# Kernel optimization log

Hardware: AMD Instinct MI355X
Metric: run time of the kernel (lower is better)

The kernel has to match this reference:

```python
import jax, jax.numpy as jnp
import numpy as np
from jax import lax


def _gru(x, h, Wih, Whh, bih, bhh):
    # PyTorch GRU cell: gates order (r, z, n)
    gi = x @ Wih.T + bih
    gh = h @ Whh.T + bhh
    ir, iz, inn = jnp.split(gi, 3, axis=-1)
    hr, hz, hn = jnp.split(gh, 3, axis=-1)
    r = jax.nn.sigmoid(ir + hr)
    z = jax.nn.sigmoid(iz + hz)
    n = jnp.tanh(inn + r * hn)
    return (1.0 - z) * n + z * h


def setup_inputs() -> dict:
    key = jax.random.key(0)
    ks = jax.random.split(key, 20)
    B, T, D, H, V, S = 128, 80, 4096, 1024, 6000, 10
    s = 0.02
    inp = {
        "data": jax.random.normal(ks[0], (B, T, D), dtype=jnp.float32),
        "mask": jnp.ones((B, S), dtype=jnp.float32),
        "target": jax.random.randint(ks[1], (B, S), 0, V),
        "sent_len": S,
        "enc_Wih": jax.random.normal(ks[2], (3 * H, D), dtype=jnp.float32) * s,
        "enc_Whh": jax.random.normal(ks[3], (3 * H, H), dtype=jnp.float32) * s,
        "enc_bih": jax.random.normal(ks[4], (3 * H,), dtype=jnp.float32) * s,
        "enc_bhh": jax.random.normal(ks[5], (3 * H,), dtype=jnp.float32) * s,
        "dec_Wih": jax.random.normal(ks[6], (3 * H, H), dtype=jnp.float32) * s,
        "dec_Whh": jax.random.normal(ks[7], (3 * H, H), dtype=jnp.float32) * s,
        "dec_bih": jax.random.normal(ks[8], (3 * H,), dtype=jnp.float32) * s,
        "dec_bhh": jax.random.normal(ks[9], (3 * H,), dtype=jnp.float32) * s,
        "lin1_W": jax.random.normal(ks[10], (H, 2 * H), dtype=jnp.float32) * s,
        "lin1_b": jnp.zeros((H,), dtype=jnp.float32),
        "lin2_W": jax.random.normal(ks[11], (V, H), dtype=jnp.float32) * s,
        "lin2_b": jnp.zeros((V,), dtype=jnp.float32),
        "embed": jax.random.normal(ks[12], (V, H), dtype=jnp.float32) * s,
    }
    return inp


def reference(data, mask, target, sent_len,
              enc_Wih, enc_Whh, enc_bih, enc_bhh,
              dec_Wih, dec_Whh, dec_bih, dec_bhh,
              lin1_W, lin1_b, lin2_W, lin2_b, embed):
    B = data.shape[0]
    H = lin1_b.shape[0]
    W1a = lin1_W[:, :H]   # acts on encoder hidden half
    W1b = lin1_W[:, H:]   # acts on embedded word half

    eh0 = jnp.zeros((B, H), dtype=data.dtype)
    dh0 = jnp.zeros((B, H), dtype=data.dtype)

    # ---- encode phase: feed video features; decoder sees [enc_hid, 0] ----
    def enc_step(carry, x_t):
        eh, dh = carry
        eh = _gru(x_t, eh, enc_Wih, enc_Whh, enc_bih, enc_bhh)
        u = jax.nn.relu(eh @ W1a.T + lin1_b)  # zeros half contributes nothing
        dh = _gru(u, dh, dec_Wih, dec_Whh, dec_bih, dec_bhh)
        return (eh, dh), None

    (eh, dh), _ = lax.scan(enc_step, (eh0, dh0), jnp.swapaxes(data, 0, 1))

    # ---- decode phase: encoder input is zeros; decoder sees [enc_hid, embed(word)] ----
    ir0, iz0, in0 = jnp.split(enc_bih, 3)  # zero-input encoder gates

    def dec_step(carry, tgt_t):
        eh, dh, word = carry
        gh = eh @ enc_Whh.T + enc_bhh
        hr, hz, hn = jnp.split(gh, 3, axis=-1)
        r = jax.nn.sigmoid(ir0 + hr)
        z = jax.nn.sigmoid(iz0 + hz)
        n = jnp.tanh(in0 + r * hn)
        eh = (1.0 - z) * n + z * eh

        emb = embed[word]  # [B, H]
        u = jax.nn.relu(eh @ W1a.T + emb @ W1b.T + lin1_b)
        dh = _gru(u, dh, dec_Wih, dec_Whh, dec_bih, dec_bhh)
        logp = jax.nn.log_softmax(dh @ lin2_W.T + lin2_b, axis=-1)  # [B, V]
        new_word = jnp.argmax(logp, axis=1).astype(jnp.int32)
        loss_t = -jnp.mean(logp[jnp.arange(B), tgt_t])  # NLLLoss (mask unused, as in source)
        return (eh, dh, new_word), (loss_t, new_word[0], new_word[1])

    word0 = jnp.ones((B,), dtype=jnp.int32)
    (_, _, _), (losses, sent, sent2) = lax.scan(dec_step, (eh, dh, word0), jnp.swapaxes(target, 0, 1))
    return jnp.sum(losses), sent, sent2
```

## Files before the change

### kernel.cpp

```cpp
#include <hip/hip_runtime.h>
#include <math.h>
#include <float.h>

#define B_ 128
#define T_ 80
#define D_ 4096
#define H_ 1024
#define V_ 6000
#define VP 6016
#define S_ 10
#define G3 (3*H_)
#define KSPLIT 4
#define NBLK 256
#define BAR_MASTER 320
#define BAR_GEN    336

typedef unsigned short ushort_t;
typedef unsigned long long ull_t;
typedef __attribute__((ext_vector_type(8))) short s16x8;
typedef __attribute__((ext_vector_type(4))) float fx4;

__device__ float    g_gi[(size_t)B_*T_*G3];
__device__ ushort_t g_Ah[(size_t)B_*T_*D_];
__device__ ushort_t g_Al[(size_t)B_*T_*D_];
__device__ ushort_t g_Bh[(size_t)G3*D_];
__device__ ushort_t g_Bl[(size_t)G3*D_];
__device__ ushort_t g_Whh_h[G3*H_],  g_Whh_l[G3*H_];
__device__ ushort_t g_dWih_h[G3*H_], g_dWih_l[G3*H_];
__device__ ushort_t g_dWhh_h[G3*H_], g_dWhh_l[G3*H_];
__device__ ushort_t g_l1h[H_*2*H_],  g_l1l[H_*2*H_];
__device__ ushort_t g_l2h[(size_t)VP*H_], g_l2l[(size_t)VP*H_];
__device__ float g_ghp [KSPLIT*B_*G3];
__device__ float g_gi2p[KSPLIT*B_*G3];
__device__ float g_gh2p[KSPLIT*B_*G3];
__device__ float g_up  [KSPLIT*B_*H_];
__device__ float g_eh[B_*H_];
__device__ float g_dh[B_*H_];
__device__ ushort_t g_ehh[B_*H_], g_ehl[B_*H_];
__device__ ushort_t g_dhh[B_*H_], g_dhl[B_*H_];
__device__ ushort_t g_uh[B_*H_],  g_ul[B_*H_];
__device__ ushort_t g_cath[B_*2*H_], g_catl[B_*2*H_];
__device__ float g_logitsp[2*B_*VP];
__device__ int   g_word[B_];
__device__ int   g_bar[512];

__device__ __forceinline__ ull_t ald64(const void* p) {
    return __hip_atomic_load((const ull_t*)p, __ATOMIC_RELAXED, __HIP_MEMORY_SCOPE_AGENT);
}
__device__ __forceinline__ void ast64(void* p, ull_t v) {
    __hip_atomic_store((ull_t*)p, v, __ATOMIC_RELAXED, __HIP_MEMORY_SCOPE_AGENT);
}
__device__ __forceinline__ unsigned ald32(const void* p) {
    return __hip_atomic_load((const unsigned*)p, __ATOMIC_RELAXED, __HIP_MEMORY_SCOPE_AGENT);
}
__device__ __forceinline__ void ast32(void* p, unsigned v) {
    __hip_atomic_store((unsigned*)p, v, __ATOMIC_RELAXED, __HIP_MEMORY_SCOPE_AGENT);
}
__device__ __forceinline__ void astf(float* p, float v) {
    ast32(p, __float_as_uint(v));
}
__device__ __forceinline__ float2 u2f2(ull_t v) {
    union { ull_t u; float2 f; } x; x.u = v; return x.f;
}
__device__ __forceinline__ s16x8 ald_s16x8(const ushort_t* p) {
    union { ull_t q[2]; s16x8 v; } u;
    u.q[0] = ald64(p); u.q[1] = ald64(p + 4);
    return u.v;
}

__device__ __forceinline__ void split1(float x, ushort_t& hi, ushort_t& lo) {
    unsigned u = __float_as_uint(x);
    unsigned rh = u + 0x7FFF + ((u >> 16) & 1);
    hi = (ushort_t)(rh >> 16);
    float fhi = __uint_as_float((unsigned)hi << 16);
    float d = x - fhi;
    unsigned u2 = __float_as_uint(d);
    unsigned rl = u2 + 0x7FFF + ((u2 >> 16) & 1);
    lo = (ushort_t)(rl >> 16);
}

__global__ __launch_bounds__(256) void split_bf16(
    const float* __restrict__ x, ushort_t* __restrict__ hi,
    ushort_t* __restrict__ lo, int n4)
{
    int i = blockIdx.x * 256 + threadIdx.x;
    if (i >= n4) return;
    float4 v = ((const float4*)x)[i];
    ushort_t h0,h1,h2,h3,l0,l1,l2,l3;
    split1(v.x,h0,l0); split1(v.y,h1,l1); split1(v.z,h2,l2); split1(v.w,h3,l3);
    ushort_t* hp = hi + (size_t)i*4;  hp[0]=h0; hp[1]=h1; hp[2]=h2; hp[3]=h3;
    ushort_t* lp = lo + (size_t)i*4;  lp[0]=l0; lp[1]=l1; lp[2]=l2; lp[3]=l3;
}

__device__ __forceinline__ void gld16(const ushort_t* g, void* l) {
    __builtin_amdgcn_global_load_lds(
        (const __attribute__((address_space(1))) void*)(const void*)g,
        (__attribute__((address_space(3))) void*)l, 16, 0, 0);
}

__device__ __forceinline__ float gru_elem(float ir,float iz,float inn,
                                          float hr,float hz,float hn,float hprev){
    const float r = 1.f/(1.f+expf(-(ir+hr)));
    const float z = 1.f/(1.f+expf(-(iz+hz)));
    const float n = tanhf(inn + r*hn);
    return (1.f-z)*n + z*hprev;
}

__global__ __launch_bounds__(256) void gemm_x3(
    const ushort_t* __restrict__ Ah, const ushort_t* __restrict__ Al, int lda,
    const ushort_t* __restrict__ Bh, const ushort_t* __restrict__ Bl, int ldw,
    const float* __restrict__ bias,
    float* __restrict__ C,
    int M, int N, int K, int kchunks,
    const ushort_t* __restrict__ A2h, const ushort_t* __restrict__ A2l,
    const ushort_t* __restrict__ B2h, const ushort_t* __restrict__ B2l,
    float* __restrict__ C2)
{
    int z = blockIdx.z;
    int kc = z;
    if (z >= kchunks) { kc = z - kchunks; Ah=A2h; Al=A2l; Bh=B2h; Bl=B2l; C=C2; }

    __shared__ ushort_t sAh[2][128*32], sAl[2][128*32];
    __shared__ ushort_t sBh[2][128*32], sBl[2][128*32];

    const int tid  = threadIdx.x;
    const int bm   = blockIdx.y * 128, bn = blockIdx.x * 128;
    const int wave = tid >> 6, lane = tid & 63;
    const int wr   = (wave >> 1) * 64, wc = (wave & 1) * 64;
    const int r    = lane & 15, g = lane >> 4;

    fx4 acc[4][4] = {};

    const int kper = K / kchunks;
    const int kbeg = kc * kper;
    const int nt   = kper / 32;

#define STAGE(buf, k0)                                                        \
    {                                                                         \
      _Pragma("unroll")                                                       \
      for (int i_ = 0; i_ < 2; ++i_) {                                        \
        const int o_   = (tid + i_*256) * 16;                                 \
        const int row_ = o_ >> 6;                                             \
        const int el_  = (o_ & 63) >> 1;                                      \
        const size_t ga_ = (size_t)(bm + row_) * lda + (k0) + el_;            \
        const size_t gb_ = (size_t)(bn + row_) * ldw + (k0) + el_;            \
        const int lb_ = (wave*64 + i_*256) * 16;                              \
        gld16(Ah + ga_, (char*)&sAh[buf][0] + lb_);                           \
        gld16(Al + ga_, (char*)&sAl[buf][0] + lb_);                           \
        gld16(Bh + gb_, (char*)&sBh[buf][0] + lb_);                           \
        gld16(Bl + gb_, (char*)&sBl[buf][0] + lb_);                           \
      }                                                                       \
    }

    int cur = 0;
    STAGE(0, kbeg)
    __syncthreads();

    for (int t = 0; t < nt; ++t) {
        if (t + 1 < nt) STAGE(cur ^ 1, kbeg + (t+1)*32)

        s16x8 a_h[4], a_l[4], b_h[4], b_l[4];
#pragma unroll
        for (int i = 0; i < 4; ++i) {
            const int ao = (wr + i*16 + r)*32 + g*8;
            const int bo = (wc + i*16 + r)*32 + g*8;
            a_h[i] = *(const s16x8*)&sAh[cur][ao];
            a_l[i] = *(const s16x8*)&sAl[cur][ao];
            b_h[i] = *(const s16x8*)&sBh[cur][bo];
            b_l[i] = *(const s16x8*)&sBl[cur][bo];
        }
#pragma unroll
        for (int i = 0; i < 4; ++i)
#pragma unroll
            for (int j = 0; j < 4; ++j) {
                acc[i][j] = __builtin_amdgcn_mfma_f32_16x16x32_bf16(a_h[i], b_h[j], acc[i][j], 0, 0, 0);
                acc[i][j] = __builtin_amdgcn_mfma_f32_16x16x32_bf16(a_l[i], b_h[j], acc[i][j], 0, 0, 0);
                acc[i][j] = __builtin_amdgcn_mfma_f32_16x16x32_bf16(a_h[i], b_l[j], acc[i][j], 0, 0, 0);
            }
        __syncthreads();
        cur ^= 1;
    }
#undef STAGE

    float* Cw = C + (size_t)kc * M * N;
#pragma unroll
    for (int i = 0; i < 4; ++i)
#pragma unroll
        for (int j = 0; j < 4; ++j)
#pragma unroll
            for (int reg = 0; reg < 4; ++reg) {
                const int row = bm + wr + i*16 + g*4 + reg;
                const int col = bn + wc + j*16 + r;
                float v = acc[i][j][reg];
                if (kchunks == 1 && bias) v += bias[col];
                Cw[(size_t)row * N + col] = v;
            }
}


__device__ __forceinline__ void cwrite_at(const fx4 (&acc)[4][4],
    float* __restrict__ Cw, int ldc, int colbase, int wr, int wc, int r, int g)
{
#pragma unroll
    for (int i = 0; i < 4; ++i)
#pragma unroll
        for (int j = 0; j < 4; ++j)
#pragma unroll
            for (int reg = 0; reg < 4; ++reg)
                astf(&Cw[(size_t)(wr + i*16 + g*4 + reg) * ldc + colbase + wc + j*16 + r],
                     acc[i][j][reg]);
}

__device__ __forceinline__ void job_resB(
    const ushort_t* __restrict__ Agh, const ushort_t* __restrict__ Agl,
    const ushort_t* __restrict__ sWh, const ushort_t* __restrict__ sWl,
    int kbeg, float* __restrict__ Cw, int ldc, int colbase)
{
    const int tid  = threadIdx.x;
    const int wave = tid >> 6, lane = tid & 63;
    const int wr   = (wave >> 1) * 64, wc = (wave & 1) * 64;
    const int r    = lane & 15, g = lane >> 4;
    fx4 acc[4][4] = {};

    s16x8 a_h[2][4], a_l[2][4];
#pragma unroll
    for (int i = 0; i < 4; ++i) {
        const size_t off = (size_t)(wr + i*16 + r) * H_ + kbeg + g*8;
        a_h[0][i] = ald_s16x8(Agh + off);
        a_l[0][i] = ald_s16x8(Agl + off);
    }
    for (int kt = 0; kt < 8; ++kt) {
        const int cur = kt & 1, nxt = cur ^ 1;
        if (kt < 7) {
#pragma unroll
            for (int i = 0; i < 4; ++i) {
                const size_t off = (size_t)(wr + i*16 + r) * H_ + kbeg + (kt+1)*32 + g*8;
                a_h[nxt][i] = ald_s16x8(Agh + off);
                a_l[nxt][i] = ald_s16x8(Agl + off);
            }
        }
        s16x8 b_h[4], b_l[4];
#pragma unroll
        for (int j = 0; j < 4; ++j) {
            const int bo = (kt*128 + (wc + j*16 + r))*32 + g*8;
            b_h[j] = *(const s16x8*)&sWh[bo];
            b_l[j] = *(const s16x8*)&sWl[bo];
        }
#pragma unroll
        for (int i = 0; i < 4; ++i)
#pragma unroll
            for (int j = 0; j < 4; ++j) {
                acc[i][j] = __builtin_amdgcn_mfma_f32_16x16x32_bf16(a_h[cur][i], b_h[j], acc[i][j], 0, 0, 0);
                acc[i][j] = __builtin_amdgcn_mfma_f32_16x16x32_bf16(a_l[cur][i], b_h[j], acc[i][j], 0, 0, 0);
                acc[i][j] = __builtin_amdgcn_mfma_f32_16x16x32_bf16(a_h[cur][i], b_l[j], acc[i][j], 0, 0, 0);
            }
    }
    cwrite_at(acc, Cw, ldc, colbase, wr, wc, r, g);
}

__device__ __forceinline__ void job_stream(
    const ushort_t* __restrict__ Agh, const ushort_t* __restrict__ Agl,
    const ushort_t* __restrict__ Wgh, const ushort_t* __restrict__ Wgl,
    int kbeg, float* __restrict__ Cw, int ldc, int colbase)
{
    const int tid  = threadIdx.x;
    const int wave = tid >> 6, lane = tid & 63;
    const int wr   = (wave >> 1) * 64, wc = (wave & 1) * 64;
    const int r    = lane & 15, g = lane >> 4;
    fx4 acc[4][4] = {};

    s16x8 a_h[2][4], a_l[2][4], b_h[2][4], b_l[2][4];
#pragma unroll
    for (int i = 0; i < 4; ++i) {
        const size_t aoff = (size_t)(wr + i*16 + r) * H_ + kbeg + g*8;
        const size_t boff = (size_t)(wc + i*16 + r) * H_ + kbeg + g*8;
        a_h[0][i] = ald_s16x8(Agh + aoff);
        a_l[0][i] = ald_s16x8(Agl + aoff);
        b_h[0][i] = *(const s16x8*)(Wgh + boff);
        b_l[0][i] = *(const s16x8*)(Wgl + boff);
    }
    for (int kt = 0; kt < 8; ++kt) {
        const int cur = kt & 1, nxt = cur ^ 1;
        if (kt < 7) {
#pragma unroll
            for (int i = 0; i < 4; ++i) {
                const size_t aoff = (size_t)(wr + i*16 + r) * H_ + kbeg + (kt+1)*32 + g*8;
                const size_t boff = (size_t)(wc + i*16 + r) * H_ + kbeg + (kt+1)*32 + g*8;
                a_h[nxt][i] = ald_s16x8(Agh + aoff);
                a_l[nxt][i] = ald_s16x8(Agl + aoff);
                b_h[nxt][i] = *(const s16x8*)(Wgh + boff);
                b_l[nxt][i] = *(const s16x8*)(Wgl + boff);
            }
        }
#pragma unroll
        for (int i = 0; i < 4; ++i)
#pragma unroll
            for (int j = 0; j < 4; ++j) {
                acc[i][j] = __builtin_amdgcn_mfma_f32_16x16x32_bf16(a_h[cur][i], b_h[cur][j], acc[i][j], 0, 0, 0);
                acc[i][j] = __builtin_amdgcn_mfma_f32_16x16x32_bf16(a_l[cur][i], b_h[cur][j], acc[i][j], 0, 0, 0);
                acc[i][j] = __builtin_amdgcn_mfma_f32_16x16x32_bf16(a_h[cur][i], b_l[cur][j], acc[i][j], 0, 0, 0);
            }
    }
    cwrite_at(acc, Cw, ldc, colbase, wr, wc, r, g);
}

__device__ __forceinline__ void gbar(int* bar, int* lg) {
    __syncthreads();
    if (threadIdx.x == 0) {
        const int g = *lg;
        const int grp = blockIdx.x >> 4;
        const int p1 = __hip_atomic_fetch_add(&bar[grp*16], 1, __ATOMIC_RELAXED,
                                              __HIP_MEMORY_SCOPE_AGENT);
        if (p1 == 15) {
            const int p2 = __hip_atomic_fetch_add(&bar[BAR_MASTER], 1, __ATOMIC_RELAXED,
                                                  __HIP_MEMORY_SCOPE_AGENT);
            if (p2 == 15) {
                for (int g2 = 0; g2 < 16; ++g2)
                    __hip_atomic_store(&bar[g2*16], 0, __ATOMIC_RELAXED, __HIP_MEMORY_SCOPE_AGENT);
                __hip_atomic_store(&bar[BAR_MASTER], 0, __ATOMIC_RELAXED, __HIP_MEMORY_SCOPE_AGENT);
                __hip_atomic_store(&bar[BAR_GEN], g + 1, __ATOMIC_RELAXED, __HIP_MEMORY_SCOPE_AGENT);
            } else {
                while (__hip_atomic_load(&bar[BAR_GEN], __ATOMIC_RELAXED,
                                         __HIP_MEMORY_SCOPE_AGENT) == g)
                    __builtin_amdgcn_s_sleep(2);
            }
        } else {
            while (__hip_atomic_load(&bar[BAR_GEN], __ATOMIC_RELAXED,
                                     __HIP_MEMORY_SCOPE_AGENT) == g)
                __builtin_amdgcn_s_sleep(2);
        }
        *lg = g + 1;
    }
    __syncthreads();
}

__device__ __forceinline__ void dec_update2(int base,
    const float* __restrict__ gi2p, const float* __restrict__ gh2p,
    const float* __restrict__ dec_bih, const float* __restrict__ dec_bhh,
    float* __restrict__ dh, ushort_t* __restrict__ dhh, ushort_t* __restrict__ dhl)
{
    const int b = base >> 10, j = base & (H_ - 1);
    float2 ir = *(const float2*)&dec_bih[j];
    float2 iz = *(const float2*)&dec_bih[H_+j];
    float2 in2 = *(const float2*)&dec_bih[2*H_+j];
    const float* p = gi2p + (size_t)b * G3;
#pragma unroll
    for (int s2 = 0; s2 < KSPLIT; ++s2) {
        float2 a0 = u2f2(ald64(&p[j]));      ir.x += a0.x; ir.y += a0.y;
        float2 a1 = u2f2(ald64(&p[H_+j]));   iz.x += a1.x; iz.y += a1.y;
        float2 a2 = u2f2(ald64(&p[2*H_+j])); in2.x += a2.x; in2.y += a2.y;
        p += (size_t)B_ * G3;
    }
    float2 hr = *(const float2*)&dec_bhh[j];
    float2 hz = *(const float2*)&dec_bhh[H_+j];
    float2 hn = *(const float2*)&dec_bhh[2*H_+j];
    const float* q = gh2p + (size_t)b * G3;
#pragma unroll
    for (int s2 = 0; s2 < KSPLIT; ++s2) {
        float2 a0 = u2f2(ald64(&q[j]));      hr.x += a0.x; hr.y += a0.y;
        float2 a1 = u2f2(ald64(&q[H_+j]));   hz.x += a1.x; hz.y += a1.y;
        float2 a2 = u2f2(ald64(&q[2*H_+j])); hn.x += a2.x; hn.y += a2.y;
        q += (size_t)B_ * G3;
    }
    float2 old = *(const float2*)&dh[base];
    const float v0 = gru_elem(ir.x, iz.x, in2.x, hr.x, hz.x, hn.x, old.x);
    const float v1 = gru_elem(ir.y, iz.y, in2.y, hr.y, hz.y, hn.y, old.y);
    *(float2*)&dh[base] = make_float2(v0, v1);
    ushort_t h0,l0,h1,l1;
    split1(v0,h0,l0); split1(v1,h1,l1);
    ast32(&dhh[base], (unsigned)h0 | ((unsigned)h1 << 16));
    ast32(&dhl[base], (unsigned)l0 | ((unsigned)l1 << 16));
}

__global__ __launch_bounds__(256) void enc_persist(
    const float* __restrict__ gi,
    const ushort_t* __restrict__ Whh_h, const ushort_t* __restrict__ Whh_l,
    const ushort_t* __restrict__ l1h,   const ushort_t* __restrict__ l1l,
    const ushort_t* __restrict__ dWih_h,const ushort_t* __restrict__ dWih_l,
    const ushort_t* __restrict__ dWhh_h,const ushort_t* __restrict__ dWhh_l,
    const float* __restrict__ enc_bhh,  const float* __restrict__ lin1_b,
    const float* __restrict__ dec_bih,  const float* __restrict__ dec_bhh,
    float* __restrict__ eh, ushort_t* __restrict__ ehh, ushort_t* __restrict__ ehl,
    float* __restrict__ dh, ushort_t* __restrict__ dhh, ushort_t* __restrict__ dhl,
    ushort_t* __restrict__ uh, ushort_t* __restrict__ ul,
    float* __restrict__ ghp, float* __restrict__ up,
    float* __restrict__ gi2p, float* __restrict__ gh2p,
    int* __restrict__ bar)
{
    extern __shared__ ushort_t smw[];
    ushort_t* sWh = smw;
    ushort_t* sWl = smw + 32768;

    const int bid = blockIdx.x;
    const int tid = threadIdx.x;
    int lg = 0;

    if (bid < 224) {
        const ushort_t *Wh, *Wl; int ldw, rowbase, kbeg0;
        if (bid < 96)       { const int jj=bid;     Wh=Whh_h;  Wl=Whh_l;  ldw=H_;   rowbase=(jj>>2)*128; kbeg0=(jj&3)*256; }
        else if (bid < 128) { const int jj=bid-96;  Wh=l1h;    Wl=l1l;    ldw=2*H_; rowbase=(jj>>2)*128; kbeg0=(jj&3)*256; }
        else                { const int jj=bid-128; Wh=dWhh_h; Wl=dWhh_l; ldw=H_;   rowbase=(jj>>2)*128; kbeg0=(jj&3)*256; }
        for (int c = tid; c < 4096; c += 256) {
            const int row  = c >> 5;
            const int col8 = (c & 31) * 8;
            const int kt = col8 >> 5, kk = col8 & 31;
            const size_t goff = (size_t)(rowbase + row) * ldw + kbeg0 + col8;
            const int    loff = (kt*128 + row)*32 + kk;
            *(s16x8*)&sWh[loff] = *(const s16x8*)(Wh + goff);
            *(s16x8*)&sWl[loff] = *(const s16x8*)(Wl + goff);
        }
    }
    __syncthreads();

    for (int t = 0; t < T_; ++t) {
        {
            const int base = bid * 512 + tid * 2;
            const int b = base >> 10, j = base & (H_ - 1);
            const float* girow = gi + ((size_t)(b * T_ + t)) * G3;
            float2 ir = *(const float2*)&girow[j];
            float2 iz = *(const float2*)&girow[H_+j];
            float2 in2 = *(const float2*)&girow[2*H_+j];
            float2 hr = *(const float2*)&enc_bhh[j];
            float2 hz = *(const float2*)&enc_bhh[H_+j];
            float2 hn = *(const float2*)&enc_bhh[2*H_+j];
            const float* q = ghp + (size_t)b * G3;
#pragma unroll
            for (int s2 = 0; s2 < KSPLIT; ++s2) {
                float2 a0 = u2f2(ald64(&q[j]));      hr.x += a0.x; hr.y += a0.y;
                float2 a1 = u2f2(ald64(&q[H_+j]));   hz.x += a1.x; hz.y += a1.y;
                float2 a2 = u2f2(ald64(&q[2*H_+j])); hn.x += a2.x; hn.y += a2.y;
                q += (size_t)B_ * G3;
            }
            float2 old = *(const float2*)&eh[base];
            const float v0 = gru_elem(ir.x, iz.x, in2.x, hr.x, hz.x, hn.x, old.x);
            const float v1 = gru_elem(ir.y, iz.y, in2.y, hr.y, hz.y, hn.y, old.y);
            *(float2*)&eh[base] = make_float2(v0, v1);
            ushort_t h0,l0,h1,l1;
            split1(v0,h0,l0); split1(v1,h1,l1);
            ast32(&ehh[base], (unsigned)h0 | ((unsigned)h1 << 16));
            ast32(&ehl[base], (unsigned)l0 | ((unsigned)l1 << 16));
            if (t > 0)
                dec_update2(base, gi2p, gh2p, dec_bih, dec_bhh, dh, dhh, dhl);
        }
        gbar(bar, &lg);

        if (bid < 96) {
            const int ntile = bid >> 2, kc = bid & 3;
            job_resB(ehh, ehl, sWh, sWl, kc*256,
                     ghp + (size_t)kc * B_ * G3, G3, ntile * 128);
        } else if (bid < 128) {
            const int jj = bid - 96, ntile = jj >> 2, kc = jj & 3;
            job_resB(ehh, ehl, sWh, sWl, kc*256,
                     up + (size_t)kc * B_ * H_, H_, ntile * 128);
        } else if (bid < 224) {
            const int jj = bid - 128, ntile = jj >> 2, kc = jj & 3;
            job_resB(dhh, dhl, sWh, sWl, kc*256,
                     gh2p + (size_t)kc * B_ * G3, G3, ntile * 128);
        }
        gbar(bar, &lg);

        {
            const int base = bid * 512 + tid * 2;
            const int j = base & (H_ - 1);
            float2 v = *(const float2*)&lin1_b[j];
#pragma unroll
            for (int s2 = 0; s2 < KSPLIT; ++s2) {
                float2 a = u2f2(ald64(&up[(size_t)s2 * B_ * H_ + base]));
                v.x += a.x; v.y += a.y;
            }
            v.x = fmaxf(v.x, 0.f); v.y = fmaxf(v.y, 0.f);
            ushort_t h0,l0,h1,l1;
            split1(v.x,h0,l0); split1(v.y,h1,l1);
            ast32(&uh[base], (unsigned)h0 | ((unsigned)h1 << 16));
            ast32(&ul[base], (unsigned)l0 | ((unsigned)l1 << 16));
        }
        gbar(bar, &lg);

        if (bid < 96) {
            const int ntile = bid >> 2, kc = bid & 3;
            job_stream(uh, ul,
                       dWih_h + (size_t)ntile * 128 * H_,
                       dWih_l + (size_t)ntile * 128 * H_,
                       kc * 256,
                       gi2p + (size_t)kc * B_ * G3, G3, ntile * 128);
        }
        gbar(bar, &lg);
    }

    {
        const int base = bid * 512 + tid * 2;
        dec_update2(base, gi2p, gh2p, dec_bih, dec_bhh, dh, dhh, dhl);
    }
}

__global__ __launch_bounds__(256) void gru_update2(
    const float* __restrict__ GI, int gi_rstride, int gi_nsplit,
    const float* __restrict__ bih,
    const float* __restrict__ GHp, const float* __restrict__ bhh,
    float* __restrict__ h, ushort_t* __restrict__ hh, ushort_t* __restrict__ hl)
{
    const int idx = blockIdx.x * 256 + threadIdx.x;
    const int b = idx >> 10;
    const int j = idx & (H_ - 1);
    float ir, iz, inn;
    if (gi_nsplit == 0) {
        const float* gi = GI + (size_t)b * gi_rstride;
        ir = gi[j]; iz = gi[H_ + j]; inn = gi[2*H_ + j];
    } else {
        ir = bih[j]; iz = bih[H_ + j]; inn = bih[2*H_ + j];
        const float* p = GI + (size_t)b * G3;
#pragma unroll
        for (int s = 0; s < KSPLIT; ++s) {
            ir += p[j]; iz += p[H_ + j]; inn += p[2*H_ + j];
            p += (size_t)B_ * G3;
        }
    }
    float hr = bhh[j], hz = bhh[H_ + j], hn = bhh[2*H_ + j];
    const float* q = GHp + (size_t)b * G3;
#pragma unroll
    for (int s = 0; s < KSPLIT; ++s) {
        hr += q[j]; hz += q[H_ + j]; hn += q[2*H_ + j];
        q += (size_t)B_ * G3;
    }
    const float v = gru_elem(ir, iz, inn, hr, hz, hn, h[idx]);
    h[idx] = v;
    split1(v, hh[idx], hl[idx]);
}

__global__ __launch_bounds__(256) void relu_combine(
    const float* __restrict__ Up, const float* __restrict__ bias,
    ushort_t* __restrict__ uh, ushort_t* __restrict__ ul)
{
    const int idx = blockIdx.x * 256 + threadIdx.x;
    const int j = idx & (H_ - 1);
    float v = bias[j];
#pragma unroll
    for (int s = 0; s < KSPLIT; ++s) v += Up[(size_t)s * B_ * H_ + idx];
    v = fmaxf(v, 0.f);
    split1(v, uh[idx], ul[idx]);
}

__global__ __launch_bounds__(256) void cat_eh_emb(
    const ushort_t* __restrict__ ehh, const ushort_t* __restrict__ ehl,
    const float* __restrict__ embed, const int* __restrict__ word,
    ushort_t* __restrict__ cath, ushort_t* __restrict__ catl)
{
    const int idx = blockIdx.x * 256 + threadIdx.x;
    const int b = idx >> 11;
    const int j = idx & (2*H_ - 1);
    if (j < H_) {
        cath[idx] = ehh[b * H_ + j];
        catl[idx] = ehl[b * H_ + j];
    } else {
        float v = embed[(size_t)word[b] * H_ + (j - H_)];
        split1(v, cath[idx], catl[idx]);
    }
}

__global__ __launch_bounds__(256) void init_state(
    float* __restrict__ eh, float* __restrict__ dh,
    ushort_t* __restrict__ ehh, ushort_t* __restrict__ ehl,
    ushort_t* __restrict__ dhh, ushort_t* __restrict__ dhl,
    int* __restrict__ word, float* __restrict__ out,
    float* __restrict__ ghp, int* __restrict__ bar)
{
    const int idx = blockIdx.x * 256 + threadIdx.x;
    if (idx < KSPLIT*B_*G3) ghp[idx] = 0.f;
    if (idx < B_*H_) {
        eh[idx] = 0.f; dh[idx] = 0.f;
        ehh[idx] = 0; ehl[idx] = 0; dhh[idx] = 0; dhl[idx] = 0;
    }
    if (idx < B_)   word[idx] = 1;
    if (idx < 21)   out[idx] = 0.f;
    if (idx < 512)  bar[idx] = 0;
}

__global__ __launch_bounds__(256) void softmax_loss(
    const float* __restrict__ logp, const float* __restrict__ l2b,
    const int* __restrict__ target, int s, int* __restrict__ word,
    float* __restrict__ out)
{
    const int b = blockIdx.x;
    const int t = threadIdx.x;
    const float* p0 = logp + (size_t)b * VP;
    const float* p1 = p0 + (size_t)B_ * VP;
    __shared__ float sv[256];
    __shared__ int   si[256];
    __shared__ float ss[256];

    float best = -FLT_MAX; int bi = 0;
    for (int j = t; j < V_; j += 256) {
        float v = p0[j] + p1[j] + l2b[j];
        if (v > best) { best = v; bi = j; }
    }
    sv[t] = best; si[t] = bi;
    __syncthreads();
    for (int off = 128; off > 0; off >>= 1) {
        if (t < off) {
            float v2 = sv[t + off]; int i2 = si[t + off];
            if (v2 > sv[t] || (v2 == sv[t] && i2 < si[t])) { sv[t] = v2; si[t] = i2; }
        }
        __syncthreads();
    }
    const float m = sv[0];
    const int amax = si[0];

    float sum = 0.f;
    for (int j = t; j < V_; j += 256) sum += expf(p0[j] + p1[j] + l2b[j] - m);
    ss[t] = sum;
    __syncthreads();
    for (int off = 128; off > 0; off >>= 1) {
        if (t < off) ss[t] += ss[t + off];
        __syncthreads();
    }
    if (t == 0) {
        const float lse = m + logf(ss[0]);
        const int tgt = target[b * S_ + s];
        const float logit_t = p0[tgt] + p1[tgt] + l2b[tgt];
        atomicAdd(&out[0], -(logit_t - lse) * (1.0f / (float)B_));
        word[b] = amax;
        if (b == 0) out[1 + s]  = (float)amax;
        if (b == 1) out[11 + s] = (float)amax;
    }
}

static inline void launch_x3(hipStream_t st,
    const ushort_t* Ah, const ushort_t* Al, int lda,
    const ushort_t* Bh, const ushort_t* Bl, int ldw,
    const float* bias, float* C, int M, int N, int K, int kchunks)
{
    dim3 grid(N/128, M/128, kchunks);
    gemm_x3<<<grid, 256, 0, st>>>(Ah, Al, lda, Bh, Bl, ldw, bias, C, M, N, K, kchunks,
                                  nullptr, nullptr, nullptr, nullptr, nullptr);
}

static inline void launch_x3_dual(hipStream_t st,
    const ushort_t* Ah, const ushort_t* Al,
    const ushort_t* Bh, const ushort_t* Bl, float* C,
    const ushort_t* A2h, const ushort_t* A2l,
    const ushort_t* B2h, const ushort_t* B2l, float* C2,
    int M, int N, int K, int kchunks)
{
    dim3 grid(N/128, M/128, 2*kchunks);
    gemm_x3<<<grid, 256, 0, st>>>(Ah, Al, H_, Bh, Bl, H_, nullptr, C, M, N, K, kchunks,
                                  A2h, A2l, B2h, B2l, C2);
}

extern "C" void kernel_launch(void* const* d_in, const int* in_sizes, int n_in,
                              void* d_out, int out_size, void* d_ws, size_t ws_size,
                              hipStream_t stream)
{
    const float* data    = (const float*)d_in[0];
    const int*   target  = (const int*)  d_in[2];
    const float* enc_Wih = (const float*)d_in[4];
    const float* enc_Whh = (const float*)d_in[5];
    const float* enc_bih = (const float*)d_in[6];
    const float* enc_bhh = (const float*)d_in[7];
    const float* dec_Wih = (const float*)d_in[8];
    const float* dec_Whh = (const float*)d_in[9];
    const float* dec_bih = (const float*)d_in[10];
    const float* dec_bhh = (const float*)d_in[11];
    const float* lin1_W  = (const float*)d_in[12];
    const float* lin1_b  = (const float*)d_in[13];
    const float* lin2_W  = (const float*)d_in[14];
    const float* lin2_b  = (const float*)d_in[15];
    const float* embed   = (const float*)d_in[16];
    float* out = (float*)d_out;

    float *gi, *eh, *dh, *logitsp, *ghp, *gi2p, *gh2p, *up;
    ushort_t *Ah, *Al, *Bh, *Bl, *Whh_h, *Whh_l, *dWih_h, *dWih_l, *dWhh_h, *dWhh_l;
    ushort_t *l1h, *l1l, *l2h, *l2l, *ehh, *ehl, *dhh, *dhl, *uh, *ul, *cath, *catl;
    int *word, *bar;
    hipGetSymbolAddress((void**)&gi,     HIP_SYMBOL(g_gi));
    hipGetSymbolAddress((void**)&Ah,     HIP_SYMBOL(g_Ah));
    hipGetSymbolAddress((void**)&Al,     HIP_SYMBOL(g_Al));
    hipGetSymbolAddress((void**)&Bh,     HIP_SYMBOL(g_Bh));
    hipGetSymbolAddress((void**)&Bl,     HIP_SYMBOL(g_Bl));
    hipGetSymbolAddress((void**)&Whh_h,  HIP_SYMBOL(g_Whh_h));
    hipGetSymbolAddress((void**)&Whh_l,  HIP_SYMBOL(g_Whh_l));
    hipGetSymbolAddress((void**)&dWih_h, HIP_SYMBOL(g_dWih_h));
    hipGetSymbolAddress((void**)&dWih_l, HIP_SYMBOL(g_dWih_l));
    hipGetSymbolAddress((void**)&dWhh_h, HIP_SYMBOL(g_dWhh_h));
    hipGetSymbolAddress((void**)&dWhh_l, HIP_SYMBOL(g_dWhh_l));
    hipGetSymbolAddress((void**)&l1h,    HIP_SYMBOL(g_l1h));
    hipGetSymbolAddress((void**)&l1l,    HIP_SYMBOL(g_l1l));
    hipGetSymbolAddress((void**)&l2h,    HIP_SYMBOL(g_l2h));
    hipGetSymbolAddress((void**)&l2l,    HIP_SYMBOL(g_l2l));
    hipGetSymbolAddress((void**)&ghp,    HIP_SYMBOL(g_ghp));
    hipGetSymbolAddress((void**)&gi2p,   HIP_SYMBOL(g_gi2p));
    hipGetSymbolAddress((void**)&gh2p,   HIP_SYMBOL(g_gh2p));
    hipGetSymbolAddress((void**)&up,     HIP_SYMBOL(g_up));
    hipGetSymbolAddress((void**)&eh,     HIP_SYMBOL(g_eh));
    hipGetSymbolAddress((void**)&dh,     HIP_SYMBOL(g_dh));
    hipGetSymbolAddress((void**)&ehh,    HIP_SYMBOL(g_ehh));
    hipGetSymbolAddress((void**)&ehl,    HIP_SYMBOL(g_ehl));
    hipGetSymbolAddress((void**)&dhh,    HIP_SYMBOL(g_dhh));
    hipGetSymbolAddress((void**)&dhl,    HIP_SYMBOL(g_dhl));
    hipGetSymbolAddress((void**)&uh,     HIP_SYMBOL(g_uh));
    hipGetSymbolAddress((void**)&ul,     HIP_SYMBOL(g_ul));
    hipGetSymbolAddress((void**)&cath,   HIP_SYMBOL(g_cath));
    hipGetSymbolAddress((void**)&catl,   HIP_SYMBOL(g_catl));
    hipGetSymbolAddress((void**)&logitsp,HIP_SYMBOL(g_logitsp));
    hipGetSymbolAddress((void**)&word,   HIP_SYMBOL(g_word));
    hipGetSymbolAddress((void**)&bar,    HIP_SYMBOL(g_bar));

    hipFuncSetAttribute((const void*)enc_persist,
                        hipFuncAttributeMaxDynamicSharedMemorySize, 131072);

    init_state<<<6144, 256, 0, stream>>>(eh, dh, ehh, ehl, dhh, dhl, word, out, ghp, bar);

    split_bf16<<<(B_*T_*D_/4 + 255)/256, 256, 0, stream>>>(data,    Ah, Al, B_*T_*D_/4);
    split_bf16<<<(G3*D_/4   + 255)/256, 256, 0, stream>>>(enc_Wih, Bh, Bl, G3*D_/4);
    split_bf16<<<(G3*H_/4   + 255)/256, 256, 0, stream>>>(enc_Whh, Whh_h, Whh_l, G3*H_/4);
    split_bf16<<<(G3*H_/4   + 255)/256, 256, 0, stream>>>(dec_Wih, dWih_h, dWih_l, G3*H_/4);
    split_bf16<<<(G3*H_/4   + 255)/256, 256, 0, stream>>>(dec_Whh, dWhh_h, dWhh_l, G3*H_/4);
    split_bf16<<<(H_*2*H_/4 + 255)/256, 256, 0, stream>>>(lin1_W,  l1h, l1l, H_*2*H_/4);
    split_bf16<<<(V_*H_/4   + 255)/256, 256, 0, stream>>>(lin2_W,  l2h, l2l, V_*H_/4);

    launch_x3(stream, Ah, Al, D_, Bh, Bl, D_, enc_bih, gi, B_*T_, G3, D_, 1);

    enc_persist<<<NBLK, 256, 131072, stream>>>(
        gi, Whh_h, Whh_l, l1h, l1l, dWih_h, dWih_l, dWhh_h, dWhh_l,
        enc_bhh, lin1_b, dec_bih, dec_bhh,
        eh, ehh, ehl, dh, dhh, dhl, uh, ul,
        ghp, up, gi2p, gh2p, bar);

    for (int s = 0; s < S_; ++s) {
        launch_x3(stream, ehh, ehl, H_, Whh_h, Whh_l, H_, nullptr, ghp, B_, G3, H_, KSPLIT);
        gru_update2<<<512, 256, 0, stream>>>(enc_bih, 0, 0, nullptr,
                                             ghp, enc_bhh, eh, ehh, ehl);
        cat_eh_emb<<<1024, 256, 0, stream>>>(ehh, ehl, embed, word, cath, catl);
        launch_x3(stream, cath, catl, 2*H_, l1h, l1l, 2*H_, nullptr, up, B_, H_, 2*H_, KSPLIT);
        relu_combine<<<512, 256, 0, stream>>>(up, lin1_b, uh, ul);
        launch_x3_dual(stream, uh, ul, dWih_h, dWih_l, gi2p,
                               dhh, dhl, dWhh_h, dWhh_l, gh2p, B_, G3, H_, KSPLIT);
        gru_update2<<<512, 256, 0, stream>>>(gi2p, 0, KSPLIT, dec_bih,
                                             gh2p, dec_bhh, dh, dhh, dhl);
        launch_x3(stream, dhh, dhl, H_, l2h, l2l, H_, nullptr, logitsp, B_, VP, H_, 2);
        softmax_loss<<<B_, 256, 0, stream>>>(logitsp, lin2_b, target, s, word, out);
    }
}
```

Measured before the change: 8.786 ms.

## Stream recurrent weights from global in persistent encoder with 8-wave row tiles

Drops the per-block LDS cache of recurrent weight slices in the persistent encoder kernel. Each timestep the weights are now re-read from global memory, and the two GEMM job routines are replaced by one job8 routine. The block grows to 512 threads, and each of its 8 waves computes a 16x128 output strip rather than a 64x64 tile. This removes the 128KB shared-memory setup and may raise occupancy and shorten per-wave MFMA chains. In exchange, every wave re-reads the full weight tile each step, so weight traffic through cache and global memory grows a lot.

Result: slower. 12.26 ms (+39.5%).

```diff
diff --git a/kernel.cpp b/kernel.cpp
--- a/kernel.cpp
+++ b/kernel.cpp
@@ -47,12 +47,6 @@
 __device__ __forceinline__ ull_t ald64(const void* p) {
     return __hip_atomic_load((const ull_t*)p, __ATOMIC_RELAXED, __HIP_MEMORY_SCOPE_AGENT);
 }
-__device__ __forceinline__ void ast64(void* p, ull_t v) {
-    __hip_atomic_store((ull_t*)p, v, __ATOMIC_RELAXED, __HIP_MEMORY_SCOPE_AGENT);
-}
-__device__ __forceinline__ unsigned ald32(const void* p) {
-    return __hip_atomic_load((const unsigned*)p, __ATOMIC_RELAXED, __HIP_MEMORY_SCOPE_AGENT);
-}
 __device__ __forceinline__ void ast32(void* p, unsigned v) {
     __hip_atomic_store((unsigned*)p, v, __ATOMIC_RELAXED, __HIP_MEMORY_SCOPE_AGENT);
 }
@@ -197,111 +191,54 @@
             }
 }
 
-
-__device__ __forceinline__ void cwrite_at(const fx4 (&acc)[4][4],
-    float* __restrict__ Cw, int ldc, int colbase, int wr, int wc, int r, int g)
-{
-#pragma unroll
-    for (int i = 0; i < 4; ++i)
-#pragma unroll
-        for (int j = 0; j < 4; ++j)
-#pragma unroll
-            for (int reg = 0; reg < 4; ++reg)
-                astf(&Cw[(size_t)(wr + i*16 + g*4 + reg) * ldc + colbase + wc + j*16 + r],
-                     acc[i][j][reg]);
-}
-
-__device__ __forceinline__ void job_resB(
+__device__ __forceinline__ void job8(
     const ushort_t* __restrict__ Agh, const ushort_t* __restrict__ Agl,
-    const ushort_t* __restrict__ sWh, const ushort_t* __restrict__ sWl,
-    int kbeg, float* __restrict__ Cw, int ldc, int colbase)
+    const ushort_t* __restrict__ Wgh, const ushort_t* __restrict__ Wgl,
+    int ldw, int kbeg,
+    float* __restrict__ Cw, int ldc, int colbase)
 {
     const int tid  = threadIdx.x;
     const int wave = tid >> 6, lane = tid & 63;
-    const int wr   = (wave >> 1) * 64, wc = (wave & 1) * 64;
+    const int wrow = wave * 16;
     const int r    = lane & 15, g = lane >> 4;
-    fx4 acc[4][4] = {};
-
-    s16x8 a_h[2][4], a_l[2][4];
-#pragma unroll
-    for (int i = 0; i < 4; ++i) {
-        const size_t off = (size_t)(wr + i*16 + r) * H_ + kbeg + g*8;
-        a_h[0][i] = ald_s16x8(Agh + off);
-        a_l[0][i] = ald_s16x8(Agl + off);
+    fx4 acc[8] = {};
+
+    const size_t arow = (size_t)(wrow + r) * H_;
+
+    s16x8 a_h[2], a_l[2], b_h[2][8], b_l[2][8];
+    a_h[0] = ald_s16x8(Agh + arow + kbeg + g*8);
+    a_l[0] = ald_s16x8(Agl + arow + kbeg + g*8);
+#pragma unroll
+    for (int j = 0; j < 8; ++j) {
+        const size_t boff = (size_t)(colbase + j*16 + r) * ldw + kbeg + g*8;
+        b_h[0][j] = *(const s16x8*)(Wgh + boff);
+        b_l[0][j] = *(const s16x8*)(Wgl + boff);
     }
     for (int kt = 0; kt < 8; ++kt) {
         const int cur = kt & 1, nxt = cur ^ 1;
         if (kt < 7) {
-#pragma unroll
-            for (int i = 0; i < 4; ++i) {
-                const size_t off = (size_t)(wr + i*16 + r) * H_ + kbeg + (kt+1)*32 + g*8;
-                a_h[nxt][i] = ald_s16x8(Agh + off);
-                a_l[nxt][i] = ald_s16x8(Agl + off);
+            const int k0 = kbeg + (kt+1)*32;
+            a_h[nxt] = ald_s16x8(Agh + arow + k0 + g*8);
+            a_l[nxt] = ald_s16x8(Agl + arow + k0 + g*8);
+#pragma unroll
+            for (int j = 0; j < 8; ++j) {
+                const size_t boff = (size_t)(colbase + j*16 + r) * ldw + k0 + g*8;
+                b_h[nxt][j] = *(const s16x8*)(Wgh + boff);
+                b_l[nxt][j] = *(const s16x8*)(Wgl + boff);
             }
         }
-        s16x8 b_h[4], b_l[4];
-#pragma unroll
-        for (int j = 0; j < 4; ++j) {
-            const int bo = (kt*128 + (wc + j*16 + r))*32 + g*8;
-            b_h[j] = *(const s16x8*)&sWh[bo];
-            b_l[j] = *(const s16x8*)&sWl[bo];
-        }
-#pragma unroll
-        for (int i = 0; i < 4; ++i)
-#pragma unroll
-            for (int j = 0; j < 4; ++j) {
-                acc[i][j] = __builtin_amdgcn_mfma_f32_16x16x32_bf16(a_h[cur][i], b_h[j], acc[i][j], 0, 0, 0);
-                acc[i][j] = __builtin_amdgcn_mfma_f32_16x16x32_bf16(a_l[cur][i], b_h[j], acc[i][j], 0, 0, 0);
-                acc[i][j] = __builtin_amdgcn_mfma_f32_16x16x32_bf16(a_h[cur][i], b_l[j], acc[i][j], 0, 0, 0);
-            }
-    }
-    cwrite_at(acc, Cw, ldc, colbase, wr, wc, r, g);
-}
-
-__device__ __forceinline__ void job_stream(
-    const ushort_t* __restrict__ Agh, const ushort_t* __restrict__ Agl,
-    const ushort_t* __restrict__ Wgh, const ushort_t* __restrict__ Wgl,
-    int kbeg, float* __restrict__ Cw, int ldc, int colbase)
-{
-    const int tid  = threadIdx.x;
-    const int wave = tid >> 6, lane = tid & 63;
-    const int wr   = (wave >> 1) * 64, wc = (wave & 1) * 64;
-    const int r    = lane & 15, g = lane >> 4;
-    fx4 acc[4][4] = {};
-
-    s16x8 a_h[2][4], a_l[2][4], b_h[2][4], b_l[2][4];
-#pragma unroll
-    for (int i = 0; i < 4; ++i) {
-        const size_t aoff = (size_t)(wr + i*16 + r) * H_ + kbeg + g*8;
-        const size_t boff = (size_t)(wc + i*16 + r) * H_ + kbeg + g*8;
-        a_h[0][i] = ald_s16x8(Agh + aoff);
-        a_l[0][i] = ald_s16x8(Agl + aoff);
-        b_h[0][i] = *(const s16x8*)(Wgh + boff);
-        b_l[0][i] = *(const s16x8*)(Wgl + boff);
-    }
-    for (int kt = 0; kt < 8; ++kt) {
-        const int cur = kt & 1, nxt = cur ^ 1;
-        if (kt < 7) {
-#pragma unroll
-            for (int i = 0; i < 4; ++i) {
-                const size_t aoff = (size_t)(wr + i*16 + r) * H_ + kbeg + (kt+1)*32 + g*8;
-                const size_t boff = (size_t)(wc + i*16 + r) * H_ + kbeg + (kt+1)*32 + g*8;
-                a_h[nxt][i] = ald_s16x8(Agh + aoff);
-                a_l[nxt][i] = ald_s16x8(Agl + aoff);
-                b_h[nxt][i] = *(const s16x8*)(Wgh + boff);
-                b_l[nxt][i] = *(const s16x8*)(Wgl + boff);
-            }
-        }
-#pragma unroll
-        for (int i = 0; i < 4; ++i)
-#pragma unroll
-            for (int j = 0; j < 4; ++j) {
-                acc[i][j] = __builtin_amdgcn_mfma_f32_16x16x32_bf16(a_h[cur][i], b_h[cur][j], acc[i][j], 0, 0, 0);
-                acc[i][j] = __builtin_amdgcn_mfma_f32_16x16x32_bf16(a_l[cur][i], b_h[cur][j], acc[i][j], 0, 0, 0);
-                acc[i][j] = __builtin_amdgcn_mfma_f32_16x16x32_bf16(a_h[cur][i], b_l[cur][j], acc[i][j], 0, 0, 0);
-            }
-    }
-    cwrite_at(acc, Cw, ldc, colbase, wr, wc, r, g);
+#pragma unroll
+        for (int j = 0; j < 8; ++j) {
+            acc[j] = __builtin_amdgcn_mfma_f32_16x16x32_bf16(a_h[cur], b_h[cur][j], acc[j], 0, 0, 0);
+            acc[j] = __builtin_amdgcn_mfma_f32_16x16x32_bf16(a_l[cur], b_h[cur][j], acc[j], 0, 0, 0);
+            acc[j] = __builtin_amdgcn_mfma_f32_16x16x32_bf16(a_h[cur], b_l[cur][j], acc[j], 0, 0, 0);
+        }
+    }
+#pragma unroll
+    for (int j = 0; j < 8; ++j)
+#pragma unroll
+        for (int reg = 0; reg < 4; ++reg)
+            astf(&Cw[(size_t)(wrow + g*4 + reg) * ldc + colbase + j*16 + r], acc[j][reg]);
 }
 
 __device__ __forceinline__ void gbar(int* bar, int* lg) {
@@ -372,7 +309,7 @@
     ast32(&dhl[base], (unsigned)l0 | ((unsigned)l1 << 16));
 }
 
-__global__ __launch_bounds__(256) void enc_persist(
+__global__ __launch_bounds__(512) void enc_persist(
     const float* __restrict__ gi,
     const ushort_t* __restrict__ Whh_h, const ushort_t* __restrict__ Whh_l,
     const ushort_t* __restrict__ l1h,   const ushort_t* __restrict__ l1l,
@@ -387,33 +324,12 @@
     float* __restrict__ gi2p, float* __restrict__ gh2p,
     int* __restrict__ bar)
 {
-    extern __shared__ ushort_t smw[];
-    ushort_t* sWh = smw;
-    ushort_t* sWl = smw + 32768;
-
     const int bid = blockIdx.x;
     const int tid = threadIdx.x;
     int lg = 0;
 
-    if (bid < 224) {
-        const ushort_t *Wh, *Wl; int ldw, rowbase, kbeg0;
-        if (bid < 96)       { const int jj=bid;     Wh=Whh_h;  Wl=Whh_l;  ldw=H_;   rowbase=(jj>>2)*128; kbeg0=(jj&3)*256; }
-        else if (bid < 128) { const int jj=bid-96;  Wh=l1h;    Wl=l1l;    ldw=2*H_; rowbase=(jj>>2)*128; kbeg0=(jj&3)*256; }
-        else                { const int jj=bid-128; Wh=dWhh_h; Wl=dWhh_l; ldw=H_;   rowbase=(jj>>2)*128; kbeg0=(jj&3)*256; }
-        for (int c = tid; c < 4096; c += 256) {
-            const int row  = c >> 5;
-            const int col8 = (c & 31) * 8;
-            const int kt = col8 >> 5, kk = col8 & 31;
-            const size_t goff = (size_t)(rowbase + row) * ldw + kbeg0 + col8;
-            const int    loff = (kt*128 + row)*32 + kk;
-            *(s16x8*)&sWh[loff] = *(const s16x8*)(Wh + goff);
-            *(s16x8*)&sWl[loff] = *(const s16x8*)(Wl + goff);
-        }
-    }
-    __syncthreads();
-
     for (int t = 0; t < T_; ++t) {
-        {
+        if (tid < 256) {
             const int base = bid * 512 + tid * 2;
             const int b = base >> 10, j = base & (H_ - 1);
             const float* girow = gi + ((size_t)(b * T_ + t)) * G3;
@@ -446,20 +362,20 @@
 
         if (bid < 96) {
             const int ntile = bid >> 2, kc = bid & 3;
-            job_resB(ehh, ehl, sWh, sWl, kc*256,
-                     ghp + (size_t)kc * B_ * G3, G3, ntile * 128);
+            job8(ehh, ehl, Whh_h, Whh_l, H_, kc*256,
+                 ghp + (size_t)kc * B_ * G3, G3, ntile * 128);
         } else if (bid < 128) {
             const int jj = bid - 96, ntile = jj >> 2, kc = jj & 3;
-            job_resB(ehh, ehl, sWh, sWl, kc*256,
-                     up + (size_t)kc * B_ * H_, H_, ntile * 128);
+            job8(ehh, ehl, l1h, l1l, 2*H_, kc*256,
+                 up + (size_t)kc * B_ * H_, H_, ntile * 128);
         } else if (bid < 224) {
             const int jj = bid - 128, ntile = jj >> 2, kc = jj & 3;
-            job_resB(dhh, dhl, sWh, sWl, kc*256,
-                     gh2p + (size_t)kc * B_ * G3, G3, ntile * 128);
+            job8(dhh, dhl, dWhh_h, dWhh_l, H_, kc*256,
+                 gh2p + (size_t)kc * B_ * G3, G3, ntile * 128);
         }
         gbar(bar, &lg);
 
-        {
+        if (tid < 256) {
             const int base = bid * 512 + tid * 2;
             const int j = base & (H_ - 1);
             float2 v = *(const float2*)&lin1_b[j];
@@ -478,16 +394,13 @@
 
         if (bid < 96) {
             const int ntile = bid >> 2, kc = bid & 3;
-            job_stream(uh, ul,
-                       dWih_h + (size_t)ntile * 128 * H_,
-                       dWih_l + (size_t)ntile * 128 * H_,
-                       kc * 256,
-                       gi2p + (size_t)kc * B_ * G3, G3, ntile * 128);
+            job8(uh, ul, dWih_h, dWih_l, H_, kc*256,
+                 gi2p + (size_t)kc * B_ * G3, G3, ntile * 128);
         }
         gbar(bar, &lg);
     }
 
-    {
+    if (tid < 256) {
         const int base = bid * 512 + tid * 2;
         dec_update2(base, gi2p, gh2p, dec_bih, dec_bhh, dh, dhh, dhl);
     }
@@ -704,9 +617,6 @@
     hipGetSymbolAddress((void**)&word,   HIP_SYMBOL(g_word));
     hipGetSymbolAddress((void**)&bar,    HIP_SYMBOL(g_bar));
 
-    hipFuncSetAttribute((const void*)enc_persist,
-                        hipFuncAttributeMaxDynamicSharedMemorySize, 131072);
-
     init_state<<<6144, 256, 0, stream>>>(eh, dh, ehh, ehl, dhh, dhl, word, out, ghp, bar);
 
     split_bf16<<<(B_*T_*D_/4 + 255)/256, 256, 0, stream>>>(data,    Ah, Al, B_*T_*D_/4);
@@ -719,7 +629,7 @@
 
     launch_x3(stream, Ah, Al, D_, Bh, Bl, D_, enc_bih, gi, B_*T_, G3, D_, 1);
 
-    enc_persist<<<NBLK, 256, 131072, stream>>>(
+    enc_persist<<<NBLK, 512, 0, stream>>>(
         gi, Whh_h, Whh_l, l1h, l1l, dWih_h, dWih_l, dWhh_h, dWhh_l,
         enc_bhh, lin1_b, dec_bih, dec_bhh,
         eh, ehh, ehl, dh, dhh, dhl, uh, ul,
```
